# Kernel tuning notes

Hardware: AMD Instinct MI355X
Metric: run time of the kernel (lower is better)

## Reference

```python
import math
import jax, jax.numpy as jnp
import numpy as np

B, S, D, H, F = 2, 2048, 1024, 16, 4096
HD = D // H
EPS = 1e-6
ALPHA, BETA = 0.5, 1.0  # SpectralActivation defaults


def setup_inputs() -> dict:
    key = jax.random.key(0)
    ks = jax.random.split(key, 24)
    init = lambda k, shape: (jax.random.normal(k, shape, jnp.float32) * 0.02)
    return {
        "x": jax.random.normal(ks[0], (B, S, D), jnp.float32),
        # attention params (W stored as [in, out], i.e. y = x @ W + b)
        "Wq": init(ks[1], (D, D)), "bq": jnp.zeros((D,), jnp.float32),
        "Wk": init(ks[2], (D, D)), "bk": jnp.zeros((D,), jnp.float32),
        "Wv": init(ks[3], (D, D)), "bv": jnp.zeros((D,), jnp.float32),
        "Wo": init(ks[4], (D, D)), "bo": jnp.zeros((D,), jnp.float32),
        "resonance": jnp.ones((H, 1, 1), jnp.float32),
        "phase": jnp.zeros((H, 1, 1), jnp.float32),
        # norm1
        "g1": jnp.ones((D,), jnp.float32), "b1": jnp.zeros((D,), jnp.float32),
        "s1": jnp.full((1,), 0.1, jnp.float32),
        # FFN
        "W1": init(ks[5], (D, F)), "bf1": jnp.zeros((F,), jnp.float32),
        "W2": init(ks[6], (F, D)), "bf2": jnp.zeros((D,), jnp.float32),
        # norm2
        "g2": jnp.ones((D,), jnp.float32), "b2": jnp.zeros((D,), jnp.float32),
        "s2": jnp.full((1,), 0.1, jnp.float32),
    }


def _harmonic_ln(x, gamma, beta, stab):
    mean = jnp.mean(x, axis=-1, keepdims=True)
    std = jnp.std(x, axis=-1, keepdims=True, ddof=1)  # torch std is unbiased
    std = std + stab * jnp.sin(std * math.pi)
    return gamma * ((x - mean) / (std + EPS)) + beta


def _spectral_act(x):
    c = math.sqrt(2.0 / math.pi)
    gelu_like = 0.5 * x * (1.0 + jnp.tanh(c * (x + 0.044715 * x ** 3)))
    return gelu_like + ALPHA * jnp.sin(BETA * x)


def _forward(x, Wq, bq, Wk, bk, Wv, bv, Wo, bo, resonance, phase,
             g1, b1, s1, W1, bf1, W2, bf2, g2, b2, s2):
    Bq, Sq, _ = x.shape
    q = (x @ Wq + bq).reshape(Bq, Sq, H, HD).transpose(0, 2, 1, 3)  # [B,H,S,hd]
    k = (x @ Wk + bk).reshape(Bq, Sq, H, HD).transpose(0, 2, 1, 3)
    v = (x @ Wv + bv).reshape(Bq, Sq, H, HD).transpose(0, 2, 1, 3)

    scores = jnp.einsum('bhqd,bhkd->bhqk', q, k) / math.sqrt(HD)  # [B,H,S,S]
    scores = scores + resonance[None] * jnp.sin(scores + phase[None])
    attn = jax.nn.softmax(scores, axis=-1)
    out = jnp.einsum('bhqk,bhkd->bhqd', attn, v)
    out = out.transpose(0, 2, 1, 3).reshape(Bq, Sq, D)
    attn_out = out @ Wo + bo

    x = _harmonic_ln(x + attn_out, g1, b1, s1)
    ff = _spectral_act(x @ W1 + bf1) @ W2 + bf2
    x = _harmonic_ln(x + ff, g2, b2, s2)
    return x


def reference(x, Wq, bq, Wk, bk, Wv, bv, Wo, bo, resonance, phase,
              g1, b1, s1, W1, bf1, W2, bf2, g2, b2, s2):
    return _forward(x, Wq, bq, Wk, bk, Wv, bv, Wo, bo, resonance, phase,
                    g1, b1, s1, W1, bf1, W2, bf2, g2, b2, s2)
```

## Files before the change

### kernel.cpp

```cpp
#include <hip/hip_runtime.h>
#include <cstdint>
#include <cstddef>


typedef float  f32x4  __attribute__((ext_vector_type(4)));
typedef __bf16 bf16x8 __attribute__((ext_vector_type(8)));
typedef unsigned short u16x8 __attribute__((ext_vector_type(8)));
typedef unsigned short u16x4 __attribute__((ext_vector_type(4)));
typedef unsigned int   u32x2 __attribute__((ext_vector_type(2)));
typedef unsigned int   u32x4 __attribute__((ext_vector_type(4)));

#define MFMA_BF16(a, b, c) __builtin_amdgcn_mfma_f32_16x16x32_bf16((a), (b), (c), 0, 0, 0)

static __device__ __forceinline__ unsigned short f32_to_bf16(float f) {
  return __builtin_bit_cast(unsigned short, (__bf16)f);
}
static __device__ __forceinline__ bf16x8 lds_frag(const unsigned short* base, int byte) {
  return __builtin_bit_cast(bf16x8, *(const u16x8*)((const char*)base + byte));
}
static __device__ __forceinline__ float spectral_act(float x) {
  const float c = 0.7978845608028654f;
  float g = 0.5f * x * (1.0f + tanhf(c * (x + 0.044715f * x * x * x)));
  return g + 0.5f * __sinf(x);
}
static __device__ __forceinline__ void gload_lds16(const void* g, void* lds) {
  __builtin_amdgcn_global_load_lds((const __attribute__((address_space(1))) unsigned int*)g,
                                   (__attribute__((address_space(3))) unsigned int*)lds,
                                   16, 0, 0);
}
static __device__ __forceinline__ u32x2 tr_read(unsigned addr) {
  u32x2 r;
  asm volatile("ds_read_b64_tr_b16 %0, %1" : "=v"(r) : "v"(addr));
  return r;
}

__global__ __launch_bounds__(256) void cvt_f32_bf16(const float* __restrict__ in,
                                                    unsigned short* __restrict__ out, int n) {
  int i = (blockIdx.x * 256 + threadIdx.x) * 4;
  if (i < n) {
    float4 v = *(const float4*)(in + i);
    u16x4 o;
    o[0] = f32_to_bf16(v.x); o[1] = f32_to_bf16(v.y);
    o[2] = f32_to_bf16(v.z); o[3] = f32_to_bf16(v.w);
    *(u16x4*)(out + i) = o;
  }
}

__global__ __launch_bounds__(256) void transpose_f32_bf16(const float* __restrict__ W,
                                                          unsigned short* __restrict__ Wt,
                                                          int K, int N) {
  __shared__ float tile[32][33];
  int tx = threadIdx.x & 31, ty = threadIdx.x >> 5;
  int k0 = blockIdx.y * 32, n0 = blockIdx.x * 32;
#pragma unroll
  for (int i = 0; i < 4; i++)
    tile[ty + i * 8][tx] = W[(size_t)(k0 + ty + i * 8) * N + n0 + tx];
  __syncthreads();
#pragma unroll
  for (int i = 0; i < 4; i++)
    Wt[(size_t)(n0 + ty + i * 8) * K + k0 + tx] = f32_to_bf16(tile[tx][ty + i * 8]);
}

template <int BM, int BN, int EPI>
__global__ __launch_bounds__(256) void gemm_bt(const unsigned short* __restrict__ A,
                                               const unsigned short* __restrict__ Bt,
                                               const float* __restrict__ bias,
                                               unsigned short* __restrict__ Cb,
                                               float* __restrict__ Cf,
                                               int M, int N, int K) {
  constexpr int MI = BM / 32;
  constexpr int NI = BN / 32;
  __shared__ unsigned short As[BM * 32];
  __shared__ unsigned short Bs[BN * 32];
  const int t = threadIdx.x;
  const int lane = t & 63, w = t >> 6;
  const int wr = w >> 1, wc = w & 1;
  const int g = lane >> 4, cc = lane & 15;
  const int row0 = blockIdx.y * BM, col0 = blockIdx.x * BN;

  f32x4 acc[MI][NI];
#pragma unroll
  for (int mi = 0; mi < MI; mi++)
#pragma unroll
    for (int ni = 0; ni < NI; ni++) acc[mi][ni] = (f32x4){0.f, 0.f, 0.f, 0.f};

  const int nk = K >> 5;
  const int srow = lane >> 2;
  const int schunk = (lane & 3) ^ ((lane >> 2) & 3);

  for (int kt = 0; kt < nk; ++kt) {
#pragma unroll
    for (int i = 0; i < BM / 64; ++i) {
      int r = i * 64 + w * 16 + srow;
      gload_lds16(A + (size_t)(row0 + r) * K + (kt << 5) + schunk * 8,
                  As + (i * 64 + w * 16) * 32);
    }
#pragma unroll
    for (int i = 0; i < BN / 64; ++i) {
      int r = i * 64 + w * 16 + srow;
      gload_lds16(Bt + (size_t)(col0 + r) * K + (kt << 5) + schunk * 8,
                  Bs + (i * 64 + w * 16) * 32);
    }
    __syncthreads();

    bf16x8 af[MI], bg[NI];
#pragma unroll
    for (int mi = 0; mi < MI; mi++) {
      int r = wr * (BM / 2) + mi * 16 + cc;
      af[mi] = lds_frag(As, r * 64 + ((g ^ (cc & 3)) << 4));
    }
#pragma unroll
    for (int ni = 0; ni < NI; ni++) {
      int r = wc * (BN / 2) + ni * 16 + cc;
      bg[ni] = lds_frag(Bs, r * 64 + ((g ^ (cc & 3)) << 4));
    }
#pragma unroll
    for (int mi = 0; mi < MI; mi++)
#pragma unroll
      for (int ni = 0; ni < NI; ni++)
        acc[mi][ni] = MFMA_BF16(af[mi], bg[ni], acc[mi][ni]);
    __syncthreads();
  }

#pragma unroll
  for (int mi = 0; mi < MI; mi++) {
#pragma unroll
    for (int ni = 0; ni < NI; ni++) {
      int col = col0 + wc * (BN / 2) + ni * 16 + cc;
      float bv = bias[col];
#pragma unroll
      for (int r4 = 0; r4 < 4; r4++) {
        int row = row0 + wr * (BM / 2) + mi * 16 + g * 4 + r4;
        float val = acc[mi][ni][r4] + bv;
        if (EPI == 2) val = spectral_act(val);
        if (EPI == 0 || EPI == 2) Cb[(size_t)row * N + col] = f32_to_bf16(val);
        else                      Cf[(size_t)row * N + col] = val;
      }
    }
  }
}

__global__ __launch_bounds__(256) void attn_fused(const unsigned short* __restrict__ Qb,
                                                  const unsigned short* __restrict__ Kb,
                                                  const unsigned short* __restrict__ Vb,
                                                  int ld,
                                                  const float* __restrict__ resonance,
                                                  const float* __restrict__ phase,
                                                  unsigned short* __restrict__ O, int ldo) {
  constexpr int S = 2048;
  __shared__ unsigned short Ks[64 * 64];
  __shared__ unsigned short Vs[4][64 * 16];
  __shared__ unsigned short Ps[4][16 * 64];

  const int t = threadIdx.x, lane = t & 63, w = t >> 6;
  const int g = lane >> 4, cc = lane & 15;
  const int bh = blockIdx.y, b = bh >> 4, h = bh & 15;
  const int q0 = blockIdx.x * 64 + w * 16;
  const float res = resonance[h], ph = phase[h];

  const unsigned short* Qh = Qb + (size_t)b * S * ld + h * 64;
  const unsigned short* Kh = Kb + (size_t)b * S * ld + h * 64;
  const unsigned short* Vh = Vb + (size_t)b * S * ld + h * 64;

  bf16x8 qa0, qa1;
  {
    const unsigned short* qp = Qh + (size_t)(q0 + cc) * ld + g * 8;
    qa0 = __builtin_bit_cast(bf16x8, *(const u16x8*)qp);
    qa1 = __builtin_bit_cast(bf16x8, *(const u16x8*)(qp + 32));
  }

  bf16x8 ones8;
#pragma unroll
  for (int j = 0; j < 8; j++) ones8[j] = (__bf16)1.0f;

  const unsigned vs_base = (unsigned)(uintptr_t)(void*)&Vs[0][0];
  const unsigned tr_a = vs_base + (unsigned)((8 * g + (cc >> 2)) * 32 +
                                             (((cc & 2) >> 1) ^ (g & 1)) * 16 +
                                             (cc & 1) * 8);

  f32x4 oacc[4];
#pragma unroll
  for (int i = 0; i < 4; i++) oacc[i] = (f32x4){0.f, 0.f, 0.f, 0.f};
  float Mx[4] = {-1e30f, -1e30f, -1e30f, -1e30f};
  float Lx[4] = {0.f, 0.f, 0.f, 0.f};
  char* PsW = (char*)&Ps[w][0];

  for (int kt = 0; kt < S / 64; ++kt) {
    __syncthreads();
    {
      int r = t >> 3, c8 = (t & 7) * 8;
      const unsigned short* kp = Kh + (size_t)(kt * 64) * ld;
#pragma unroll
      for (int hh = 0; hh < 2; ++hh) {
        int row = r + hh * 32;
        u16x8 v = *(const u16x8*)(kp + (size_t)row * ld + c8);
        *(u16x8*)((char*)Ks + ((row * 128 + c8 * 2) ^ ((row & 7) << 4))) = v;
      }
      int key = t & 63, bb = t >> 6;
      const unsigned short* vp = Vh + (size_t)(kt * 64 + key) * ld + bb * 16;
      u16x8 v0 = *(const u16x8*)vp;
      u16x8 v1 = *(const u16x8*)(vp + 8);
      int sw = (key >> 3) & 1;
      char* vb = (char*)&Vs[bb][0] + key * 32;
      *(u16x8*)(vb + sw * 16) = v0;
      *(u16x8*)(vb + (1 - sw) * 16) = v1;
    }
    __syncthreads();

    f32x4 sacc[4];
#pragma unroll
    for (int nb = 0; nb < 4; nb++) sacc[nb] = (f32x4){0.f, 0.f, 0.f, 0.f};
#pragma unroll
    for (int nb = 0; nb < 4; nb++) {
      int key = nb * 16 + cc;
      int rb = key * 128, xr = (key & 7) << 4;
      bf16x8 k0 = lds_frag(Ks, (rb + g * 16) ^ xr);
      bf16x8 k1 = lds_frag(Ks, (rb + 64 + g * 16) ^ xr);
      sacc[nb] = MFMA_BF16(qa0, k0, sacc[nb]);
      sacc[nb] = MFMA_BF16(qa1, k1, sacc[nb]);
    }

    float sm[4] = {-1e30f, -1e30f, -1e30f, -1e30f};
#pragma unroll
    for (int nb = 0; nb < 4; nb++)
#pragma unroll
      for (int r4 = 0; r4 < 4; r4++) {
        float sv = sacc[nb][r4] * 0.125f;
        sv += res * __sinf(sv + ph);
        sacc[nb][r4] = sv;
        sm[r4] = fmaxf(sm[r4], sv);
      }
#pragma unroll
    for (int d = 1; d < 16; d <<= 1)
#pragma unroll
      for (int r4 = 0; r4 < 4; r4++) sm[r4] = fmaxf(sm[r4], __shfl_xor(sm[r4], d, 16));

    float alpha[4];
#pragma unroll
    for (int r4 = 0; r4 < 4; r4++) {
      float nm = fmaxf(Mx[r4], sm[r4]);
      alpha[r4] = __expf(Mx[r4] - nm);
      Mx[r4] = nm;
    }
#pragma unroll
    for (int nb = 0; nb < 4; nb++)
#pragma unroll
      for (int r4 = 0; r4 < 4; r4++) {
        float p = __expf(sacc[nb][r4] - Mx[r4]);
        int prow = g * 4 + r4, pcol = nb * 16 + cc;
        *(unsigned short*)(PsW + ((prow * 128 + pcol * 2) ^ ((prow & 7) << 4))) =
            f32_to_bf16(p);
      }

    bf16x8 pa0, pa1;
    {
      int xr = (cc & 7) << 4;
      pa0 = lds_frag((const unsigned short*)PsW, (cc * 128 + g * 16) ^ xr);
      pa1 = lds_frag((const unsigned short*)PsW, (cc * 128 + 64 + g * 16) ^ xr);
    }
    f32x4 pacc = (f32x4){0.f, 0.f, 0.f, 0.f};
    pacc = MFMA_BF16(pa0, ones8, pacc);
    pacc = MFMA_BF16(pa1, ones8, pacc);
#pragma unroll
    for (int r4 = 0; r4 < 4; r4++) Lx[r4] = Lx[r4] * alpha[r4] + pacc[r4];
#pragma unroll
    for (int nb2 = 0; nb2 < 4; nb2++)
#pragma unroll
      for (int r4 = 0; r4 < 4; r4++) oacc[nb2][r4] *= alpha[r4];

    u32x2 trv[4][4];
#pragma unroll
    for (int b2 = 0; b2 < 4; b2++) {
      unsigned a = tr_a + b2 * 2048;
      trv[b2][0] = tr_read(a);
      trv[b2][1] = tr_read(a + 128);
      trv[b2][2] = tr_read(a + 1024);
      trv[b2][3] = tr_read(a + 1152);
    }
    asm volatile("s_waitcnt lgkmcnt(0)" ::: "memory");
    __builtin_amdgcn_sched_barrier(0);
#pragma unroll
    for (int b2 = 0; b2 < 4; b2++) {
      bf16x8 v0 = __builtin_bit_cast(bf16x8,
          (u32x4){trv[b2][0][0], trv[b2][0][1], trv[b2][1][0], trv[b2][1][1]});
      bf16x8 v1 = __builtin_bit_cast(bf16x8,
          (u32x4){trv[b2][2][0], trv[b2][2][1], trv[b2][3][0], trv[b2][3][1]});
      oacc[b2] = MFMA_BF16(pa0, v0, oacc[b2]);
      oacc[b2] = MFMA_BF16(pa1, v1, oacc[b2]);
    }
  }

#pragma unroll
  for (int nb2 = 0; nb2 < 4; nb2++)
#pragma unroll
    for (int r4 = 0; r4 < 4; r4++) {
      float ov = oacc[nb2][r4] / Lx[r4];
      O[(size_t)(b * S + q0 + g * 4 + r4) * ldo + h * 64 + nb2 * 16 + cc] = f32_to_bf16(ov);
    }
}

__global__ __launch_bounds__(256) void resid_harmonic_ln(const float* __restrict__ xin,
                                                         const float* __restrict__ radd,
                                                         const float* __restrict__ gamma,
                                                         const float* __restrict__ beta,
                                                         const float* __restrict__ stab,
                                                         float* __restrict__ yf,
                                                         unsigned short* __restrict__ yb) {
  const int row = blockIdx.x, t = threadIdx.x;
  const float* xr = xin + (size_t)row * 1024;
  const float* rr = radd + (size_t)row * 1024;
  float v[4], s = 0.f, ss = 0.f;
#pragma unroll
  for (int j = 0; j < 4; j++) {
    int idx = t + j * 256;
    v[j] = xr[idx] + rr[idx];
    s += v[j]; ss += v[j] * v[j];
  }
#pragma unroll
  for (int d = 1; d < 64; d <<= 1) { s += __shfl_xor(s, d); ss += __shfl_xor(ss, d); }
  __shared__ float sb[8];
  int lane = t & 63, wid = t >> 6;
  if (lane == 0) { sb[wid] = s; sb[4 + wid] = ss; }
  __syncthreads();
  s = sb[0] + sb[1] + sb[2] + sb[3];
  ss = sb[4] + sb[5] + sb[6] + sb[7];
  float mean = s * (1.f / 1024.f);
  float var = fmaxf((ss - 1024.f * mean * mean) * (1.f / 1023.f), 0.f);
  float sd = sqrtf(var);
  sd += stab[0] * sinf(sd * 3.14159265358979323846f);
  float inv = 1.f / (sd + 1e-6f);
#pragma unroll
  for (int j = 0; j < 4; j++) {
    int idx = t + j * 256;
    float y = gamma[idx] * ((v[j] - mean) * inv) + beta[idx];
    yf[(size_t)row * 1024 + idx] = y;
    if (yb) yb[(size_t)row * 1024 + idx] = f32_to_bf16(y);
  }
}

extern "C" void kernel_launch(void* const* d_in, const int* in_sizes, int n_in,
                              void* d_out, int out_size, void* d_ws, size_t ws_size,
                              hipStream_t stream) {
  const float* x    = (const float*)d_in[0];
  const float* Wq   = (const float*)d_in[1];
  const float* bq   = (const float*)d_in[2];
  const float* Wk   = (const float*)d_in[3];
  const float* bk   = (const float*)d_in[4];
  const float* Wv   = (const float*)d_in[5];
  const float* bv   = (const float*)d_in[6];
  const float* Wo   = (const float*)d_in[7];
  const float* bo   = (const float*)d_in[8];
  const float* reso = (const float*)d_in[9];
  const float* phas = (const float*)d_in[10];
  const float* g1   = (const float*)d_in[11];
  const float* b1   = (const float*)d_in[12];
  const float* s1   = (const float*)d_in[13];
  const float* W1   = (const float*)d_in[14];
  const float* bf1  = (const float*)d_in[15];
  const float* W2   = (const float*)d_in[16];
  const float* bf2  = (const float*)d_in[17];
  const float* g2   = (const float*)d_in[18];
  const float* b2   = (const float*)d_in[19];
  const float* s2   = (const float*)d_in[20];

  const int BS = 4096;

  char* ws = (char*)d_ws;
  const size_t OFF_QKV  = 0;
  const size_t OFF_XB   = 25165824;
  const size_t OFF_WQKV = 33554432;
  const size_t OFF_WOT  = 39845888;
  const size_t OFF_W1T  = 41943040;
  const size_t OFF_W2T  = 50331648;
  const size_t OFF_BQKV = 58720256;
  const size_t OFF_T0   = 58736640;
  const size_t OFF_X1   = 75513856;
  const size_t OFF_X1B  = 92291072;

  unsigned short* qkv   = (unsigned short*)(ws + OFF_QKV);
  unsigned short* xb    = (unsigned short*)(ws + OFF_XB);
  unsigned short* ao    = (unsigned short*)(ws + OFF_XB);
  unsigned short* Wqkvt = (unsigned short*)(ws + OFF_WQKV);
  unsigned short* Wot   = (unsigned short*)(ws + OFF_WOT);
  unsigned short* W1t   = (unsigned short*)(ws + OFF_W1T);
  unsigned short* W2t   = (unsigned short*)(ws + OFF_W2T);
  float*          bqkv  = (float*)(ws + OFF_BQKV);
  float*          t0    = (float*)(ws + OFF_T0);
  float*          x1    = (float*)(ws + OFF_X1);
  unsigned short* x1b   = (unsigned short*)(ws + OFF_X1B);
  unsigned short* hb    = (unsigned short*)(ws + OFF_QKV);
  float*          out   = (float*)d_out;

  cvt_f32_bf16<<<4096, 256, 0, stream>>>(x, xb, BS * 1024);

  transpose_f32_bf16<<<dim3(32, 32), 256, 0, stream>>>(Wq, Wqkvt, 1024, 1024);
  transpose_f32_bf16<<<dim3(32, 32), 256, 0, stream>>>(Wk, Wqkvt + (size_t)1024 * 1024, 1024, 1024);
  transpose_f32_bf16<<<dim3(32, 32), 256, 0, stream>>>(Wv, Wqkvt + (size_t)2048 * 1024, 1024, 1024);
  transpose_f32_bf16<<<dim3(32, 32), 256, 0, stream>>>(Wo, Wot, 1024, 1024);
  transpose_f32_bf16<<<dim3(128, 32), 256, 0, stream>>>(W1, W1t, 1024, 4096);
  transpose_f32_bf16<<<dim3(32, 128), 256, 0, stream>>>(W2, W2t, 4096, 1024);

  hipMemcpyAsync((void*)bqkv,          (const void*)bq, 1024 * 4, hipMemcpyDeviceToDevice, stream);
  hipMemcpyAsync((void*)(bqkv + 1024), (const void*)bk, 1024 * 4, hipMemcpyDeviceToDevice, stream);
  hipMemcpyAsync((void*)(bqkv + 2048), (const void*)bv, 1024 * 4, hipMemcpyDeviceToDevice, stream);

  gemm_bt<128, 128, 0><<<dim3(24, 32), 256, 0, stream>>>(xb, Wqkvt, bqkv, qkv, nullptr,
                                                         4096, 3072, 1024);

  attn_fused<<<dim3(32, 32), 256, 0, stream>>>(qkv, qkv + 1024, qkv + 2048, 3072,
                                               reso, phas, ao, 1024);

  gemm_bt<128, 64, 1><<<dim3(16, 32), 256, 0, stream>>>(ao, Wot, bo, nullptr, t0,
                                                        4096, 1024, 1024);

  resid_harmonic_ln<<<4096, 256, 0, stream>>>(x, t0, g1, b1, s1, x1, x1b);

  gemm_bt<128, 128, 2><<<dim3(32, 32), 256, 0, stream>>>(x1b, W1t, bf1, hb, nullptr,
                                                         4096, 4096, 1024);

  gemm_bt<128, 64, 1><<<dim3(16, 32), 256, 0, stream>>>(hb, W2t, bf2, nullptr, t0,
                                                        4096, 1024, 4096);

  resid_harmonic_ln<<<4096, 256, 0, stream>>>(x1, t0, g2, b2, s2, out, nullptr);
}
```

Before: 524.7 us.

## Double-buffer GEMM LDS tiles and register-prefetch K/V in attention

The GEMM kernel now keeps two LDS buffers for the A and B tiles. It issues the async global-to-LDS loads for the next k-tile before the MFMAs of the current one, and it drops one barrier per iteration. The attention kernel prefetches the next K/V tile into registers while computing on the current tile, then writes them to LDS at the start of the next iteration. Both changes aim to hide global-memory latency behind MFMA work. In exchange, the GEMM uses twice the shared memory and the attention kernel holds more registers, both of which can reduce occupancy.

```diff
diff --git a/kernel.cpp b/kernel.cpp
--- a/kernel.cpp
+++ b/kernel.cpp
@@ -70,8 +70,8 @@
                                                int M, int N, int K) {
   constexpr int MI = BM / 32;
   constexpr int NI = BN / 32;
-  __shared__ unsigned short As[BM * 32];
-  __shared__ unsigned short Bs[BN * 32];
+  __shared__ unsigned short As[2][BM * 32];
+  __shared__ unsigned short Bs[2][BN * 32];
   const int t = threadIdx.x;
   const int lane = t & 63, w = t >> 6;
   const int wr = w >> 1, wc = w & 1;
@@ -86,40 +86,48 @@
 
   const int nk = K >> 5;
   const int srow = lane >> 2;
-  const int schunk = (lane & 3) ^ ((lane >> 2) & 3);
-
+  const int schunk = (lane & 3) ^ (srow & 3);
+
+  auto stage = [&](int buf, int kt) {
+#pragma unroll
+    for (int i = 0; i < BM / 64; ++i) {
+      int r = i * 64 + w * 16;
+      gload_lds16(A + (size_t)(row0 + r + srow) * K + (kt << 5) + schunk * 8,
+                  &As[buf][r * 32]);
+    }
+#pragma unroll
+    for (int i = 0; i < BN / 64; ++i) {
+      int r = i * 64 + w * 16;
+      gload_lds16(Bt + (size_t)(col0 + r + srow) * K + (kt << 5) + schunk * 8,
+                  &Bs[buf][r * 32]);
+    }
+  };
+
+  stage(0, 0);
+  __syncthreads();
+  int cur = 0;
   for (int kt = 0; kt < nk; ++kt) {
-#pragma unroll
-    for (int i = 0; i < BM / 64; ++i) {
-      int r = i * 64 + w * 16 + srow;
-      gload_lds16(A + (size_t)(row0 + r) * K + (kt << 5) + schunk * 8,
-                  As + (i * 64 + w * 16) * 32);
-    }
-#pragma unroll
-    for (int i = 0; i < BN / 64; ++i) {
-      int r = i * 64 + w * 16 + srow;
-      gload_lds16(Bt + (size_t)(col0 + r) * K + (kt << 5) + schunk * 8,
-                  Bs + (i * 64 + w * 16) * 32);
-    }
-    __syncthreads();
+    if (kt + 1 < nk) stage(cur ^ 1, kt + 1);
 
     bf16x8 af[MI], bg[NI];
 #pragma unroll
     for (int mi = 0; mi < MI; mi++) {
       int r = wr * (BM / 2) + mi * 16 + cc;
-      af[mi] = lds_frag(As, r * 64 + ((g ^ (cc & 3)) << 4));
+      af[mi] = lds_frag(&As[cur][0], r * 64 + ((g ^ (cc & 3)) << 4));
     }
 #pragma unroll
     for (int ni = 0; ni < NI; ni++) {
       int r = wc * (BN / 2) + ni * 16 + cc;
-      bg[ni] = lds_frag(Bs, r * 64 + ((g ^ (cc & 3)) << 4));
+      bg[ni] = lds_frag(&Bs[cur][0], r * 64 + ((g ^ (cc & 3)) << 4));
     }
 #pragma unroll
     for (int mi = 0; mi < MI; mi++)
 #pragma unroll
       for (int ni = 0; ni < NI; ni++)
         acc[mi][ni] = MFMA_BF16(af[mi], bg[ni], acc[mi][ni]);
+
     __syncthreads();
+    cur ^= 1;
   }
 
 #pragma unroll
@@ -173,6 +181,28 @@
 #pragma unroll
   for (int j = 0; j < 8; j++) ones8[j] = (__bf16)1.0f;
 
+  const int krow = t >> 3, kc8 = (t & 7) * 8;
+  const int vkey = t & 63, vb0 = (t >> 6) * 16;
+  u16x8 kr0, kr1, vr0, vr1;
+
+  auto issue_loads = [&](int kt) {
+    const unsigned short* kp = Kh + (size_t)(kt * 64) * ld;
+    kr0 = *(const u16x8*)(kp + (size_t)krow * ld + kc8);
+    kr1 = *(const u16x8*)(kp + (size_t)(krow + 32) * ld + kc8);
+    const unsigned short* vp = Vh + (size_t)(kt * 64 + vkey) * ld + vb0;
+    vr0 = *(const u16x8*)vp;
+    vr1 = *(const u16x8*)(vp + 8);
+  };
+  auto stage_lds = [&]() {
+    *(u16x8*)((char*)Ks + ((krow * 128 + kc8 * 2) ^ ((krow & 7) << 4))) = kr0;
+    int row2 = krow + 32;
+    *(u16x8*)((char*)Ks + ((row2 * 128 + kc8 * 2) ^ ((row2 & 7) << 4))) = kr1;
+    int sw = (vkey >> 3) & 1;
+    char* vb = (char*)&Vs[t >> 6][0] + vkey * 32;
+    *(u16x8*)(vb + sw * 16) = vr0;
+    *(u16x8*)(vb + (1 - sw) * 16) = vr1;
+  };
+
   const unsigned vs_base = (unsigned)(uintptr_t)(void*)&Vs[0][0];
   const unsigned tr_a = vs_base + (unsigned)((8 * g + (cc >> 2)) * 32 +
                                              (((cc & 2) >> 1) ^ (g & 1)) * 16 +
@@ -185,27 +215,11 @@
   float Lx[4] = {0.f, 0.f, 0.f, 0.f};
   char* PsW = (char*)&Ps[w][0];
 
+  issue_loads(0);
   for (int kt = 0; kt < S / 64; ++kt) {
+    stage_lds();
     __syncthreads();
-    {
-      int r = t >> 3, c8 = (t & 7) * 8;
-      const unsigned short* kp = Kh + (size_t)(kt * 64) * ld;
-#pragma unroll
-      for (int hh = 0; hh < 2; ++hh) {
-        int row = r + hh * 32;
-        u16x8 v = *(const u16x8*)(kp + (size_t)row * ld + c8);
-        *(u16x8*)((char*)Ks + ((row * 128 + c8 * 2) ^ ((row & 7) << 4))) = v;
-      }
-      int key = t & 63, bb = t >> 6;
-      const unsigned short* vp = Vh + (size_t)(kt * 64 + key) * ld + bb * 16;
-      u16x8 v0 = *(const u16x8*)vp;
-      u16x8 v1 = *(const u16x8*)(vp + 8);
-      int sw = (key >> 3) & 1;
-      char* vb = (char*)&Vs[bb][0] + key * 32;
-      *(u16x8*)(vb + sw * 16) = v0;
-      *(u16x8*)(vb + (1 - sw) * 16) = v1;
-    }
-    __syncthreads();
+    if (kt + 1 < S / 64) issue_loads(kt + 1);
 
     f32x4 sacc[4];
 #pragma unroll
@@ -288,6 +302,7 @@
       oacc[b2] = MFMA_BF16(pa0, v0, oacc[b2]);
       oacc[b2] = MFMA_BF16(pa1, v1, oacc[b2]);
     }
+    __syncthreads();
   }
 
 #pragma unroll
```

New measurement: 488.7 us. -6.9%, faster.
